# Kernel optimization log

Hardware: AMD Instinct MI355X
Metric: run time of the kernel (lower is better)

## Reference

```python
import jax, jax.numpy as jnp
import numpy as np

N = 100000      # nodes
E = 1600000     # edges (avg degree 16)
EL = 200000     # supervision (label) edges
D_IN, D_HID, D_OUT = 128, 128, 64


def setup_inputs() -> dict:
    key = jax.random.key(0)
    k = jax.random.split(key, 6)
    x = jax.random.normal(k[0], (N, D_IN), jnp.float32)
    edge_index = jax.random.randint(k[1], (2, E), 0, N, dtype=jnp.int32)
    edge_label_index = jax.random.randint(k[2], (2, EL), 0, N, dtype=jnp.int32)
    W1 = jax.random.normal(k[3], (D_IN, D_HID), jnp.float32) * (1.0 / np.sqrt(D_IN))
    b1 = jnp.zeros((D_HID,), jnp.float32)
    W2 = jax.random.normal(k[4], (D_HID, D_OUT), jnp.float32) * (1.0 / np.sqrt(D_HID))
    b2 = jnp.zeros((D_OUT,), jnp.float32)
    return {"x": x, "edge_index": edge_index, "edge_label_index": edge_label_index,
            "W1": W1, "b1": b1, "W2": W2, "b2": b2}


def gcn_layer(x, src, dst, W, b, n):
    """PyG-style GCNConv: linear -> sym-normalized scatter-add with self loops -> +bias."""
    h = x @ W                                   # [N, F]
    ones = jnp.ones(src.shape[0], h.dtype)
    deg = jax.ops.segment_sum(ones, dst, num_segments=n) + 1.0   # in-degree + self loop
    dinv = jax.lax.rsqrt(deg)                   # deg^{-1/2}
    norm = dinv[src] * dinv[dst]                # per-edge norm
    agg = jax.ops.segment_sum(h[src] * norm[:, None], dst, num_segments=n)
    agg = agg + h * (1.0 / deg)[:, None]        # self-loop contribution: dinv[i]^2
    return agg + b


def reference(x, edge_index, edge_label_index, W1, b1, W2, b2):
    src, dst = edge_index[0], edge_index[1]
    z = gcn_layer(x, src, dst, W1, b1, N)
    z = jax.nn.relu(z)                          # dropout omitted (eval mode)
    z = gcn_layer(z, src, dst, W2, b2, N)
    # decode: gather-dot over supervision edges
    return (z[edge_label_index[0]] * z[edge_label_index[1]]).sum(axis=-1)
```

## Files before the change

### kernel.cpp

```cpp
#include <hip/hip_runtime.h>
#include <stdint.h>

typedef __bf16 bf16x8 __attribute__((ext_vector_type(8)));
typedef float  floatx4 __attribute__((ext_vector_type(4)));
typedef float  floatx2 __attribute__((ext_vector_type(2)));
typedef __fp16 h2 __attribute__((ext_vector_type(2)));

__device__ __forceinline__ unsigned short f2b(float x){
    unsigned u = __float_as_uint(x);
    u = u + 0x7FFFu + ((u >> 16) & 1u);
    return (unsigned short)(u >> 16);
}
__device__ __forceinline__ float b2f(unsigned short h){
    return __uint_as_float(((unsigned)h) << 16);
}
__device__ __forceinline__ unsigned char f2f8(float x){
    int p = __builtin_amdgcn_cvt_pk_fp8_f32(x, x, 0, false);
    return (unsigned char)(p & 0xff);
}

__global__ __launch_bounds__(256) void k_scatter2(const int* __restrict__ src,
                                                  const int* __restrict__ dst,
                                                  int* __restrict__ gcur,
                                                  unsigned* __restrict__ slab,
                                                  int E_, int nbins){
    __shared__ int h[1024];
    __shared__ unsigned wbuf[4096];
    __shared__ unsigned short bbuf[4096];
    int t = threadIdx.x, blk = blockIdx.x;
    for (int i = t; i < nbins; i += 256) h[i] = 0;
    __syncthreads();
    int base = blk * 4096;
    int valid = E_ - base; if (valid > 4096) valid = 4096;
    #pragma unroll
    for (int j = 0; j < 4; j++){
        int li = (j * 256 + t) * 4;
        int e = base + li;
        if (e < E_){
            int4 d = *(const int4*)(dst + e);
            int4 s = *(const int4*)(src + e);
            wbuf[li + 0] = ((unsigned)(d.x & 127) << 25) | (unsigned)s.x;
            wbuf[li + 1] = ((unsigned)(d.y & 127) << 25) | (unsigned)s.y;
            wbuf[li + 2] = ((unsigned)(d.z & 127) << 25) | (unsigned)s.z;
            wbuf[li + 3] = ((unsigned)(d.w & 127) << 25) | (unsigned)s.w;
            bbuf[li + 0] = (unsigned short)(d.x >> 7);
            bbuf[li + 1] = (unsigned short)(d.y >> 7);
            bbuf[li + 2] = (unsigned short)(d.z >> 7);
            bbuf[li + 3] = (unsigned short)(d.w >> 7);
            atomicAdd(&h[d.x >> 7], 1);
            atomicAdd(&h[d.y >> 7], 1);
            atomicAdd(&h[d.z >> 7], 1);
            atomicAdd(&h[d.w >> 7], 1);
        }
    }
    __syncthreads();
    for (int i = t; i < nbins; i += 256){
        int hv = h[i];
        h[i] = hv ? atomicAdd(&gcur[i], hv) : 0;
    }
    __syncthreads();
    for (int i = t; i < valid; i += 256){
        int bin = bbuf[i];
        int p = atomicAdd(&h[bin], 1);
        slab[(size_t)bin * 4096 + p] = wbuf[i];
    }
}

__global__ __launch_bounds__(256) void k_binsort(const unsigned* __restrict__ slab,
                                                 const int* __restrict__ gcur,
                                                 int* __restrict__ csr,
                                                 int* __restrict__ cnt,
                                                 int* __restrict__ off,
                                                 float* __restrict__ dinv,
                                                 int n, int nbins){
    int b = blockIdx.x, t = threadIdx.x;
    __shared__ int sv[1024], sp[256];
    #pragma unroll
    for (int k = 0; k < 4; k++){
        int i = t * 4 + k;
        sv[i] = (i < nbins) ? gcur[i] : 0;
    }
    __syncthreads();
    int a0 = sv[t * 4], a1 = sv[t * 4 + 1], a2 = sv[t * 4 + 2], a3 = sv[t * 4 + 3];
    sp[t] = a0 + a1 + a2 + a3;
    __syncthreads();
    for (int o = 1; o < 256; o <<= 1){
        int v = (t >= o) ? sp[t - o] : 0;
        __syncthreads();
        sp[t] += v;
        __syncthreads();
    }
    int basep = t ? sp[t - 1] : 0;
    sv[t * 4]     = basep;
    sv[t * 4 + 1] = basep + a0;
    sv[t * 4 + 2] = basep + a0 + a1;
    sv[t * 4 + 3] = basep + a0 + a1 + a2;
    __syncthreads();
    int s0 = sv[b];
    int len = gcur[b];
    if (len > 4096) len = 4096;
    const unsigned* seg = slab + (size_t)b * 4096;
    __shared__ int cl[128], sc[128], cur[128];
    __shared__ unsigned buf[4096], outb[4096];
    if (t < 128){ cl[t] = 0; cur[t] = 0; }
    __syncthreads();
    for (int i = t; i < len; i += 256) buf[i] = seg[i];
    __syncthreads();
    for (int i = t; i < len; i += 256) atomicAdd(&cl[buf[i] >> 25], 1);
    __syncthreads();
    if (t < 128) sc[t] = cl[t];
    __syncthreads();
    for (int o = 1; o < 128; o <<= 1){
        int v = 0;
        if (t < 128 && t >= o) v = sc[t - o];
        __syncthreads();
        if (t < 128) sc[t] += v;
        __syncthreads();
    }
    for (int i = t; i < len; i += 256){
        unsigned w = buf[i];
        int nd = (int)(w >> 25);
        int p = (sc[nd] - cl[nd]) + atomicAdd(&cur[nd], 1);
        outb[p] = w & 0x1FFFFFFu;
    }
    __syncthreads();
    for (int i = t; i < len; i += 256) csr[s0 + i] = (int)outb[i];
    if (t < 128){
        int node = b * 128 + t;
        if (node < n){
            cnt[node] = cl[t];
            off[node] = s0 + (sc[t] - cl[t]);
            dinv[node] = rsqrtf((float)cl[t] + 1.0f);
        }
    }
}

__global__ __launch_bounds__(256) void k_init(const float* __restrict__ W1,
                                              const float* __restrict__ W2,
                                              unsigned short* __restrict__ wf1,
                                              unsigned* __restrict__ w2p,
                                              int* __restrict__ gcur, int nbins){
    int blk = blockIdx.x, t = threadIdx.x;
    if (blk == 24){
        for (int i = t; i < nbins; i += 256) gcur[i] = 0;
        return;
    }
    int f = blk * 256 + t;
    if (f < 2048){
        int lane = f & 63;
        int ctkc = f >> 6;
        int kc = ctkc & 3, ct = ctkc >> 2;
        int col = ct * 16 + (lane & 15);
        int k0  = kc * 32 + (lane >> 4) * 8;
        unsigned short* d = wf1 + (size_t)f * 8;
        #pragma unroll
        for (int j = 0; j < 8; j++) d[j] = f2b(W1[(k0 + j) * 128 + col]);
    } else if (f < 2048 + 4096){
        int lf = f - 2048;
        int kp = lf >> 6, lane = lf & 63;
        h2 p = __builtin_amdgcn_cvt_pkrtz(W2[(2 * kp) * 64 + lane],
                                          W2[(2 * kp + 1) * 64 + lane]);
        w2p[lf] = __builtin_bit_cast(unsigned, p);
    }
}

__global__ __launch_bounds__(256) void k_gemm1(const float* __restrict__ x,
                                               const unsigned short* __restrict__ wf,
                                               const float* __restrict__ dinv,
                                               unsigned char* __restrict__ hs, int n){
    __shared__ unsigned short Wl[16384];
    __shared__ unsigned short Al[64 * 136];
    int t = threadIdx.x;
    long rowBase = (long)blockIdx.x * 64;
    {
        const uint4* s4 = (const uint4*)wf;
        uint4* d4 = (uint4*)Wl;
        #pragma unroll
        for (int i = 0; i < 8; i++) d4[t + i * 256] = s4[t + i * 256];
    }
    {
        const float4* xs = (const float4*)(x + rowBase * 128);
        #pragma unroll
        for (int k = 0; k < 8; k++){
            int i = t + k * 256;
            int r = i >> 5, c4 = (i & 31) << 2;
            float4 v = make_float4(0.f, 0.f, 0.f, 0.f);
            if (rowBase + r < n) v = xs[i];
            unsigned lo = (unsigned)f2b(v.x) | ((unsigned)f2b(v.y) << 16);
            unsigned hi = (unsigned)f2b(v.z) | ((unsigned)f2b(v.w) << 16);
            *(uint2*)&Al[r * 136 + c4] = make_uint2(lo, hi);
        }
    }
    __syncthreads();
    int w = t >> 6, lane = t & 63, lr = lane & 15, q = lane >> 4;
    floatx4 zero = {0.f, 0.f, 0.f, 0.f};
    floatx4 acc[8];
    #pragma unroll
    for (int ct = 0; ct < 8; ct++) acc[ct] = zero;
    #pragma unroll
    for (int kc = 0; kc < 4; kc++){
        bf16x8 af = *(const bf16x8*)&Al[(w * 16 + lr) * 136 + kc * 32 + q * 8];
        #pragma unroll
        for (int ct = 0; ct < 8; ct++){
            bf16x8 bf = *(const bf16x8*)&Wl[((ct * 4 + kc) * 64 + lane) * 8];
            acc[ct] = __builtin_amdgcn_mfma_f32_16x16x32_bf16(af, bf, acc[ct], 0, 0, 0);
        }
    }
    long r0 = rowBase + w * 16 + q * 4;
    #pragma unroll
    for (int r = 0; r < 4; r++){
        long row = r0 + r;
        if (row >= n) continue;
        float dv = dinv[row];
        unsigned char* orow = hs + row * 128 + lr;
        #pragma unroll
        for (int ct = 0; ct < 8; ct++) orow[ct * 16] = f2f8(acc[ct][r] * dv);
    }
}

__global__ __launch_bounds__(256) void k_agg1g2(const unsigned char* __restrict__ hs,
                                                const int* __restrict__ off,
                                                const int* __restrict__ cnt,
                                                const int* __restrict__ csr,
                                                const float* __restrict__ dinv,
                                                const float* __restrict__ b1,
                                                const unsigned* __restrict__ w2p,
                                                unsigned short* __restrict__ hs2,
                                                int n, int nwaves){
    __shared__ unsigned W2l[4096];
    __shared__ unsigned zp[4][64];
    int t = threadIdx.x;
    {
        const uint4* w4 = (const uint4*)w2p;
        uint4* d4 = (uint4*)W2l;
        #pragma unroll
        for (int i = 0; i < 4; i++) d4[t + i * 256] = w4[t + i * 256];
    }
    __syncthreads();
    int wband = t >> 6, lane = t & 63;
    float2 bb = ((const float2*)b1)[lane];
    for (int wid = blockIdx.x * 4 + wband; wid < n; wid += nwaves){
        size_t i = (size_t)wid;
        int start = off[wid], c = cnt[wid];
        unsigned short v0 = *(const unsigned short*)(hs + i * 128 + lane * 2);
        floatx2 f0 = __builtin_amdgcn_cvt_pk_f32_fp8((int)v0, false);
        float a0 = f0.x, a1 = f0.y;
        int j = 0;
        for (; j + 8 <= c; j += 8){
            size_t s0 = (size_t)csr[start + j + 0];
            size_t s1 = (size_t)csr[start + j + 1];
            size_t s2 = (size_t)csr[start + j + 2];
            size_t s3 = (size_t)csr[start + j + 3];
            size_t s4 = (size_t)csr[start + j + 4];
            size_t s5 = (size_t)csr[start + j + 5];
            size_t s6 = (size_t)csr[start + j + 6];
            size_t s7 = (size_t)csr[start + j + 7];
            unsigned short w0 = *(const unsigned short*)(hs + s0 * 128 + lane * 2);
            unsigned short w1 = *(const unsigned short*)(hs + s1 * 128 + lane * 2);
            unsigned short w2 = *(const unsigned short*)(hs + s2 * 128 + lane * 2);
            unsigned short w3 = *(const unsigned short*)(hs + s3 * 128 + lane * 2);
            unsigned short w4 = *(const unsigned short*)(hs + s4 * 128 + lane * 2);
            unsigned short w5 = *(const unsigned short*)(hs + s5 * 128 + lane * 2);
            unsigned short w6 = *(const unsigned short*)(hs + s6 * 128 + lane * 2);
            unsigned short w7 = *(const unsigned short*)(hs + s7 * 128 + lane * 2);
            floatx2 g0 = __builtin_amdgcn_cvt_pk_f32_fp8((int)w0, false);
            floatx2 g1 = __builtin_amdgcn_cvt_pk_f32_fp8((int)w1, false);
            floatx2 g2 = __builtin_amdgcn_cvt_pk_f32_fp8((int)w2, false);
            floatx2 g3 = __builtin_amdgcn_cvt_pk_f32_fp8((int)w3, false);
            floatx2 g4 = __builtin_amdgcn_cvt_pk_f32_fp8((int)w4, false);
            floatx2 g5 = __builtin_amdgcn_cvt_pk_f32_fp8((int)w5, false);
            floatx2 g6 = __builtin_amdgcn_cvt_pk_f32_fp8((int)w6, false);
            floatx2 g7 = __builtin_amdgcn_cvt_pk_f32_fp8((int)w7, false);
            a0 += g0.x; a1 += g0.y;
            a0 += g1.x; a1 += g1.y;
            a0 += g2.x; a1 += g2.y;
            a0 += g3.x; a1 += g3.y;
            a0 += g4.x; a1 += g4.y;
            a0 += g5.x; a1 += g5.y;
            a0 += g6.x; a1 += g6.y;
            a0 += g7.x; a1 += g7.y;
        }
        for (; j < c; j++){
            size_t s = (size_t)csr[start + j];
            unsigned short v = *(const unsigned short*)(hs + s * 128 + lane * 2);
            floatx2 g = __builtin_amdgcn_cvt_pk_f32_fp8((int)v, false);
            a0 += g.x; a1 += g.y;
        }
        float dv = dinv[wid];
        float z0 = fmaxf(fmaf(dv, a0, bb.x), 0.f);
        float z1 = fmaxf(fmaf(dv, a1, bb.y), 0.f);
        zp[wband][lane] = __builtin_bit_cast(unsigned, __builtin_amdgcn_cvt_pkrtz(z0, z1));
        float acc0 = 0.f, acc1 = 0.f;
        #pragma unroll 8
        for (int kp = 0; kp < 64; kp += 2){
            h2 wa = __builtin_bit_cast(h2, W2l[kp * 64 + lane]);
            h2 wb = __builtin_bit_cast(h2, W2l[(kp + 1) * 64 + lane]);
            h2 za = __builtin_bit_cast(h2, zp[wband][kp]);
            h2 zb = __builtin_bit_cast(h2, zp[wband][kp + 1]);
            acc0 = __builtin_amdgcn_fdot2(za, wa, acc0, false);
            acc1 = __builtin_amdgcn_fdot2(zb, wb, acc1, false);
        }
        hs2[((size_t)(lane >> 3) * n + i) * 8 + (lane & 7)] = f2b((acc0 + acc1) * dv);
    }
}

__global__ __launch_bounds__(256) void k_agg2(const unsigned short* __restrict__ hs,
                                              const int* __restrict__ off,
                                              const int* __restrict__ cnt,
                                              const int* __restrict__ csr,
                                              const float* __restrict__ dinv,
                                              const float* __restrict__ b2,
                                              unsigned short* __restrict__ z2,
                                              int n, int wps){
    int t = threadIdx.x;
    int slice = blockIdx.x & 7;
    int wband = t >> 6, lane = t & 63;
    int g = lane >> 3, h = lane & 7;
    const unsigned short* tab = hs + (size_t)slice * n * 8;
    float bb = b2[slice * 8 + h];
    int wIdx = (blockIdx.x >> 3) * 4 + wband;
    int nchunks = (n + 7) >> 3;
    for (int cw = wIdx; cw < nchunks; cw += wps){
        int wid = cw * 8 + g;
        if (wid < n){
            int start = off[wid];
            int c = cnt[wid];
            float dv = dinv[wid];
            float a = b2f(tab[(size_t)wid * 8 + h]);
            int j = 0;
            for (; j + 4 <= c; j += 4){
                int s0 = csr[start + j];
                int s1 = csr[start + j + 1];
                int s2 = csr[start + j + 2];
                int s3 = csr[start + j + 3];
                unsigned short w0 = tab[(size_t)s0 * 8 + h];
                unsigned short w1 = tab[(size_t)s1 * 8 + h];
                unsigned short w2 = tab[(size_t)s2 * 8 + h];
                unsigned short w3 = tab[(size_t)s3 * 8 + h];
                a += b2f(w0); a += b2f(w1); a += b2f(w2); a += b2f(w3);
            }
            for (; j < c; j++){
                int s = csr[start + j];
                a += b2f(tab[(size_t)s * 8 + h]);
            }
            z2[(size_t)wid * 64 + slice * 8 + h] = f2b(fmaf(dv, a, bb));
        }
    }
}

__global__ __launch_bounds__(256) void k_decode(const unsigned short* __restrict__ z,
                                                const int* __restrict__ es,
                                                const int* __restrict__ et,
                                                float* __restrict__ out, int m){
    int wv = (blockIdx.x * 256 + threadIdx.x) >> 6;
    int lane = threadIdx.x & 63;
    int e = wv * 4 + (lane >> 4);
    int ql = lane & 15;
    float p = 0.f;
    if (e < m){
        size_t s = (size_t)es[e], t2 = (size_t)et[e];
        uint2 vs = *(const uint2*)(z + s * 64 + ql * 4);
        uint2 vt = *(const uint2*)(z + t2 * 64 + ql * 4);
        p = b2f((unsigned short)vs.x) * b2f((unsigned short)vt.x)
          + b2f((unsigned short)(vs.x >> 16)) * b2f((unsigned short)(vt.x >> 16))
          + b2f((unsigned short)vs.y) * b2f((unsigned short)vt.y)
          + b2f((unsigned short)(vs.y >> 16)) * b2f((unsigned short)(vt.y >> 16));
    }
    #pragma unroll
    for (int o = 8; o > 0; o >>= 1) p += __shfl_xor(p, o);
    if (ql == 0 && e < m) out[e] = p;
}


extern "C" void kernel_launch(void* const* d_in, const int* in_sizes, int n_in,
                              void* d_out, int out_size, void* d_ws, size_t ws_size,
                              hipStream_t stream){
    const float* x   = (const float*)d_in[0];
    const int*   ei  = (const int*)d_in[1];
    const int*   eli = (const int*)d_in[2];
    const float* W1  = (const float*)d_in[3];
    const float* b1  = (const float*)d_in[4];
    const float* W2  = (const float*)d_in[5];
    const float* b2  = (const float*)d_in[6];
    float* out = (float*)d_out;

    int N_  = in_sizes[0] / 128;
    int E_  = in_sizes[1] / 2;
    int EL_ = in_sizes[2] / 2;
    int NBINS = (N_ + 127) >> 7;
    const int EPB = 4096;
    int NBLK = (E_ + EPB - 1) / EPB;

    char* w = (char*)d_ws;
    size_t o = 0;
    auto alloc = [&](size_t bytes) -> size_t {
        size_t r = o; o += (bytes + 511) & ~(size_t)511; return r;
    };
    size_t o_cnt  = alloc((size_t)N_ * 4);
    size_t o_off  = alloc((size_t)N_ * 4);
    size_t o_dinv = alloc((size_t)N_ * 4);
    size_t o_gcur = alloc((size_t)NBINS * 4);
    size_t o_csr  = alloc((size_t)E_ * 4);
    size_t o_wf1  = alloc(16384 * 2);
    size_t o_w2p  = alloc(4096 * 4);
    size_t o_slab = alloc((size_t)NBINS * 4096 * 4);
    size_t o_hs1  = alloc((size_t)N_ * 128);
    size_t o_hs2  = alloc((size_t)N_ * 64 * 2);

    int* cnt  = (int*)(w + o_cnt);
    int* off  = (int*)(w + o_off);
    float* dinv = (float*)(w + o_dinv);
    int* gcur = (int*)(w + o_gcur);
    int* csr  = (int*)(w + o_csr);
    unsigned short* wf1 = (unsigned short*)(w + o_wf1);
    unsigned* w2p = (unsigned*)(w + o_w2p);
    unsigned* slab = (unsigned*)(w + o_slab);
    unsigned char* hs1 = (unsigned char*)(w + o_hs1);
    unsigned short* hs2 = (unsigned short*)(w + o_hs2);
    unsigned short* z2  = (unsigned short*)(w + o_slab);

    const int AGG1_BLOCKS = 2048;
    int nwaves = AGG1_BLOCKS * 4;
    const int AGG2_BLOCKS = 2048;
    int wps = (AGG2_BLOCKS / 8) * 4;

    k_init    <<<25, 256, 0, stream>>>(W1, W2, wf1, w2p, gcur, NBINS);
    k_scatter2<<<NBLK, 256, 0, stream>>>(ei, ei + E_, gcur, slab, E_, NBINS);
    k_binsort <<<NBINS, 256, 0, stream>>>(slab, gcur, csr, cnt, off, dinv, N_, NBINS);
    k_gemm1   <<<(N_ + 63) / 64, 256, 0, stream>>>(x, wf1, dinv, hs1, N_);
    k_agg1g2  <<<AGG1_BLOCKS, 256, 0, stream>>>(hs1, off, cnt, csr, dinv, b1, w2p, hs2, N_, nwaves);
    k_agg2    <<<AGG2_BLOCKS, 256, 0, stream>>>(hs2, off, cnt, csr, dinv, b2, z2, N_, wps);
    k_decode  <<<(EL_ + 15) / 16, 256, 0, stream>>>(z2, eli, eli + EL_, out, EL_);
}
```

Before: 300.8 us.

## Split fused agg1+GEMM2 into sliced aggregation and separate MFMA GEMM2 kernel

Aggregation for layer 1 now reads a feature-sliced fp8 table (8 slices of 16 bytes per node), so each wave handles 8 nodes per slice and keeps its gathers within a smaller table that fits cache better. The per-node fdot2 second-layer transform, previously fused into aggregation, moves into a new fp16 MFMA GEMM kernel that reads a sliced z1 buffer. CSR index loads become nontemporal, and z2 and the decode step switch to the sliced layout. This adds an extra kernel launch and a round trip of z1 through memory.

```diff
diff --git a/kernel.cpp b/kernel.cpp
--- a/kernel.cpp
+++ b/kernel.cpp
@@ -2,6 +2,7 @@
 #include <stdint.h>
 
 typedef __bf16 bf16x8 __attribute__((ext_vector_type(8)));
+typedef __fp16 f16x8 __attribute__((ext_vector_type(8)));
 typedef float  floatx4 __attribute__((ext_vector_type(4)));
 typedef float  floatx2 __attribute__((ext_vector_type(2)));
 typedef __fp16 h2 __attribute__((ext_vector_type(2)));
@@ -138,10 +139,10 @@
 __global__ __launch_bounds__(256) void k_init(const float* __restrict__ W1,
                                               const float* __restrict__ W2,
                                               unsigned short* __restrict__ wf1,
-                                              unsigned* __restrict__ w2p,
+                                              unsigned short* __restrict__ wf2,
                                               int* __restrict__ gcur, int nbins){
     int blk = blockIdx.x, t = threadIdx.x;
-    if (blk == 24){
+    if (blk == 12){
         for (int i = t; i < nbins; i += 256) gcur[i] = 0;
         return;
     }
@@ -155,12 +156,19 @@
         unsigned short* d = wf1 + (size_t)f * 8;
         #pragma unroll
         for (int j = 0; j < 8; j++) d[j] = f2b(W1[(k0 + j) * 128 + col]);
-    } else if (f < 2048 + 4096){
-        int lf = f - 2048;
-        int kp = lf >> 6, lane = lf & 63;
-        h2 p = __builtin_amdgcn_cvt_pkrtz(W2[(2 * kp) * 64 + lane],
-                                          W2[(2 * kp + 1) * 64 + lane]);
-        w2p[lf] = __builtin_bit_cast(unsigned, p);
+    } else {
+        int id = f - 2048;
+        int lane = id & 63;
+        int ctkc = id >> 6;
+        int kc = ctkc & 3, ct = ctkc >> 2;
+        int col = ct * 16 + (lane & 15);
+        int k0  = kc * 32 + (lane >> 4) * 8;
+        unsigned short* d = wf2 + (size_t)id * 8;
+        #pragma unroll
+        for (int j = 0; j < 8; j++){
+            __fp16 hv = (__fp16)W2[(k0 + j) * 64 + col];
+            d[j] = __builtin_bit_cast(unsigned short, hv);
+        }
     }
 }
 
@@ -212,95 +220,124 @@
         long row = r0 + r;
         if (row >= n) continue;
         float dv = dinv[row];
-        unsigned char* orow = hs + row * 128 + lr;
-        #pragma unroll
-        for (int ct = 0; ct < 8; ct++) orow[ct * 16] = f2f8(acc[ct][r] * dv);
-    }
-}
-
-__global__ __launch_bounds__(256) void k_agg1g2(const unsigned char* __restrict__ hs,
-                                                const int* __restrict__ off,
-                                                const int* __restrict__ cnt,
-                                                const int* __restrict__ csr,
-                                                const float* __restrict__ dinv,
-                                                const float* __restrict__ b1,
-                                                const unsigned* __restrict__ w2p,
-                                                unsigned short* __restrict__ hs2,
-                                                int n, int nwaves){
-    __shared__ unsigned W2l[4096];
-    __shared__ unsigned zp[4][64];
+        #pragma unroll
+        for (int ct = 0; ct < 8; ct++)
+            hs[((size_t)ct * n + row) * 16 + lr] = f2f8(acc[ct][r] * dv);
+    }
+}
+
+__global__ __launch_bounds__(256) void k_agg1(const unsigned char* __restrict__ hs,
+                                              const int* __restrict__ off,
+                                              const int* __restrict__ cnt,
+                                              const int* __restrict__ csr,
+                                              const float* __restrict__ dinv,
+                                              const float* __restrict__ b1,
+                                              unsigned* __restrict__ z1,
+                                              int n, int wps){
     int t = threadIdx.x;
+    int slice = blockIdx.x & 7;
+    int wband = t >> 6, lane = t & 63;
+    int g = lane >> 3, h = lane & 7;
+    const unsigned char* tab = hs + (size_t)slice * n * 16;
+    unsigned* zout = z1 + (size_t)slice * n * 8;
+    float2 bb = ((const float2*)b1)[slice * 8 + h];
+    int wIdx = (blockIdx.x >> 3) * 4 + wband;
+    int nchunks = (n + 7) >> 3;
+    for (int cw = wIdx; cw < nchunks; cw += wps){
+        int wid = cw * 8 + g;
+        if (wid < n){
+            int start = off[wid];
+            int c = cnt[wid];
+            float dv = dinv[wid];
+            unsigned short u0 = *(const unsigned short*)(tab + (size_t)wid * 16 + h * 2);
+            floatx2 f0 = __builtin_amdgcn_cvt_pk_f32_fp8((int)u0, false);
+            float a0 = f0.x, a1 = f0.y;
+            int j = 0;
+            for (; j + 4 <= c; j += 4){
+                int s0 = __builtin_nontemporal_load(csr + start + j);
+                int s1 = __builtin_nontemporal_load(csr + start + j + 1);
+                int s2 = __builtin_nontemporal_load(csr + start + j + 2);
+                int s3 = __builtin_nontemporal_load(csr + start + j + 3);
+                unsigned short w0 = *(const unsigned short*)(tab + (size_t)s0 * 16 + h * 2);
+                unsigned short w1 = *(const unsigned short*)(tab + (size_t)s1 * 16 + h * 2);
+                unsigned short w2 = *(const unsigned short*)(tab + (size_t)s2 * 16 + h * 2);
+                unsigned short w3 = *(const unsigned short*)(tab + (size_t)s3 * 16 + h * 2);
+                floatx2 g0 = __builtin_amdgcn_cvt_pk_f32_fp8((int)w0, false);
+                floatx2 g1 = __builtin_amdgcn_cvt_pk_f32_fp8((int)w1, false);
+                floatx2 g2 = __builtin_amdgcn_cvt_pk_f32_fp8((int)w2, false);
+                floatx2 g3 = __builtin_amdgcn_cvt_pk_f32_fp8((int)w3, false);
+                a0 += g0.x; a1 += g0.y;
+                a0 += g1.x; a1 += g1.y;
+                a0 += g2.x; a1 += g2.y;
+                a0 += g3.x; a1 += g3.y;
+            }
+            for (; j < c; j++){
+                int s = __builtin_nontemporal_load(csr + start + j);
+                unsigned short u = *(const unsigned short*)(tab + (size_t)s * 16 + h * 2);
+                floatx2 gg = __builtin_amdgcn_cvt_pk_f32_fp8((int)u, false);
+                a0 += gg.x; a1 += gg.y;
+            }
+            float z0 = fmaxf(fmaf(dv, a0, bb.x), 0.f);
+            float z1v = fmaxf(fmaf(dv, a1, bb.y), 0.f);
+            zout[(size_t)wid * 8 + h] =
+                __builtin_bit_cast(unsigned, __builtin_amdgcn_cvt_pkrtz(z0, z1v));
+        }
+    }
+}
+
+__global__ __launch_bounds__(256) void k_gemm2(const unsigned short* __restrict__ z1,
+                                               const unsigned short* __restrict__ wf2,
+                                               const float* __restrict__ dinv,
+                                               unsigned short* __restrict__ hs2, int n){
+    __shared__ unsigned short Wl[8192];
+    __shared__ unsigned short Al[64 * 136];
+    int t = threadIdx.x;
+    long rowBase = (long)blockIdx.x * 64;
     {
-        const uint4* w4 = (const uint4*)w2p;
-        uint4* d4 = (uint4*)W2l;
-        #pragma unroll
-        for (int i = 0; i < 4; i++) d4[t + i * 256] = w4[t + i * 256];
-    }
-    __syncthreads();
-    int wband = t >> 6, lane = t & 63;
-    float2 bb = ((const float2*)b1)[lane];
-    for (int wid = blockIdx.x * 4 + wband; wid < n; wid += nwaves){
-        size_t i = (size_t)wid;
-        int start = off[wid], c = cnt[wid];
-        unsigned short v0 = *(const unsigned short*)(hs + i * 128 + lane * 2);
-        floatx2 f0 = __builtin_amdgcn_cvt_pk_f32_fp8((int)v0, false);
-        float a0 = f0.x, a1 = f0.y;
-        int j = 0;
-        for (; j + 8 <= c; j += 8){
-            size_t s0 = (size_t)csr[start + j + 0];
-            size_t s1 = (size_t)csr[start + j + 1];
-            size_t s2 = (size_t)csr[start + j + 2];
-            size_t s3 = (size_t)csr[start + j + 3];
-            size_t s4 = (size_t)csr[start + j + 4];
-            size_t s5 = (size_t)csr[start + j + 5];
-            size_t s6 = (size_t)csr[start + j + 6];
-            size_t s7 = (size_t)csr[start + j + 7];
-            unsigned short w0 = *(const unsigned short*)(hs + s0 * 128 + lane * 2);
-            unsigned short w1 = *(const unsigned short*)(hs + s1 * 128 + lane * 2);
-            unsigned short w2 = *(const unsigned short*)(hs + s2 * 128 + lane * 2);
-            unsigned short w3 = *(const unsigned short*)(hs + s3 * 128 + lane * 2);
-            unsigned short w4 = *(const unsigned short*)(hs + s4 * 128 + lane * 2);
-            unsigned short w5 = *(const unsigned short*)(hs + s5 * 128 + lane * 2);
-            unsigned short w6 = *(const unsigned short*)(hs + s6 * 128 + lane * 2);
-            unsigned short w7 = *(const unsigned short*)(hs + s7 * 128 + lane * 2);
-            floatx2 g0 = __builtin_amdgcn_cvt_pk_f32_fp8((int)w0, false);
-            floatx2 g1 = __builtin_amdgcn_cvt_pk_f32_fp8((int)w1, false);
-            floatx2 g2 = __builtin_amdgcn_cvt_pk_f32_fp8((int)w2, false);
-            floatx2 g3 = __builtin_amdgcn_cvt_pk_f32_fp8((int)w3, false);
-            floatx2 g4 = __builtin_amdgcn_cvt_pk_f32_fp8((int)w4, false);
-            floatx2 g5 = __builtin_amdgcn_cvt_pk_f32_fp8((int)w5, false);
-            floatx2 g6 = __builtin_amdgcn_cvt_pk_f32_fp8((int)w6, false);
-            floatx2 g7 = __builtin_amdgcn_cvt_pk_f32_fp8((int)w7, false);
-            a0 += g0.x; a1 += g0.y;
-            a0 += g1.x; a1 += g1.y;
-            a0 += g2.x; a1 += g2.y;
-            a0 += g3.x; a1 += g3.y;
-            a0 += g4.x; a1 += g4.y;
-            a0 += g5.x; a1 += g5.y;
-            a0 += g6.x; a1 += g6.y;
-            a0 += g7.x; a1 += g7.y;
-        }
-        for (; j < c; j++){
-            size_t s = (size_t)csr[start + j];
-            unsigned short v = *(const unsigned short*)(hs + s * 128 + lane * 2);
-            floatx2 g = __builtin_amdgcn_cvt_pk_f32_fp8((int)v, false);
-            a0 += g.x; a1 += g.y;
-        }
-        float dv = dinv[wid];
-        float z0 = fmaxf(fmaf(dv, a0, bb.x), 0.f);
-        float z1 = fmaxf(fmaf(dv, a1, bb.y), 0.f);
-        zp[wband][lane] = __builtin_bit_cast(unsigned, __builtin_amdgcn_cvt_pkrtz(z0, z1));
-        float acc0 = 0.f, acc1 = 0.f;
-        #pragma unroll 8
-        for (int kp = 0; kp < 64; kp += 2){
-            h2 wa = __builtin_bit_cast(h2, W2l[kp * 64 + lane]);
-            h2 wb = __builtin_bit_cast(h2, W2l[(kp + 1) * 64 + lane]);
-            h2 za = __builtin_bit_cast(h2, zp[wband][kp]);
-            h2 zb = __builtin_bit_cast(h2, zp[wband][kp + 1]);
-            acc0 = __builtin_amdgcn_fdot2(za, wa, acc0, false);
-            acc1 = __builtin_amdgcn_fdot2(zb, wb, acc1, false);
-        }
-        hs2[((size_t)(lane >> 3) * n + i) * 8 + (lane & 7)] = f2b((acc0 + acc1) * dv);
+        const uint4* s4 = (const uint4*)wf2;
+        uint4* d4 = (uint4*)Wl;
+        #pragma unroll
+        for (int i = 0; i < 4; i++) d4[t + i * 256] = s4[t + i * 256];
+    }
+    {
+        #pragma unroll
+        for (int k = 0; k < 4; k++){
+            int i = t + k * 256;
+            int sl = i >> 7;
+            int node = (i >> 1) & 63;
+            int hf = i & 1;
+            long row = rowBase + node;
+            uint4 v = make_uint4(0, 0, 0, 0);
+            if (row < n) v = *(const uint4*)(z1 + ((size_t)sl * n + row) * 16 + hf * 8);
+            *(uint4*)&Al[node * 136 + sl * 16 + hf * 8] = v;
+        }
+    }
+    __syncthreads();
+    int w = t >> 6, lane = t & 63, lr = lane & 15, q = lane >> 4;
+    floatx4 zero = {0.f, 0.f, 0.f, 0.f};
+    floatx4 acc[4];
+    #pragma unroll
+    for (int ct = 0; ct < 4; ct++) acc[ct] = zero;
+    #pragma unroll
+    for (int kc = 0; kc < 4; kc++){
+        f16x8 af = *(const f16x8*)&Al[(w * 16 + lr) * 136 + kc * 32 + q * 8];
+        #pragma unroll
+        for (int ct = 0; ct < 4; ct++){
+            f16x8 bf = *(const f16x8*)&Wl[((ct * 4 + kc) * 64 + lane) * 8];
+            acc[ct] = __builtin_amdgcn_mfma_f32_16x16x32_f16(af, bf, acc[ct], 0, 0, 0);
+        }
+    }
+    long r0 = rowBase + w * 16 + q * 4;
+    #pragma unroll
+    for (int r = 0; r < 4; r++){
+        long row = r0 + r;
+        if (row >= n) continue;
+        float dv = dinv[row];
+        #pragma unroll
+        for (int ct = 0; ct < 4; ct++){
+            int f = ct * 16 + lr;
+            hs2[((size_t)(f >> 3) * n + row) * 8 + (f & 7)] = f2b(acc[ct][r] * dv);
+        }
     }
 }
 
@@ -317,6 +354,7 @@
     int wband = t >> 6, lane = t & 63;
     int g = lane >> 3, h = lane & 7;
     const unsigned short* tab = hs + (size_t)slice * n * 8;
+    unsigned short* zs = z2 + (size_t)slice * n * 8;
     float bb = b2[slice * 8 + h];
     int wIdx = (blockIdx.x >> 3) * 4 + wband;
     int nchunks = (n + 7) >> 3;
@@ -329,10 +367,10 @@
             float a = b2f(tab[(size_t)wid * 8 + h]);
             int j = 0;
             for (; j + 4 <= c; j += 4){
-                int s0 = csr[start + j];
-                int s1 = csr[start + j + 1];
-                int s2 = csr[start + j + 2];
-                int s3 = csr[start + j + 3];
+                int s0 = __builtin_nontemporal_load(csr + start + j);
+                int s1 = __builtin_nontemporal_load(csr + start + j + 1);
+                int s2 = __builtin_nontemporal_load(csr + start + j + 2);
+                int s3 = __builtin_nontemporal_load(csr + start + j + 3);
                 unsigned short w0 = tab[(size_t)s0 * 8 + h];
                 unsigned short w1 = tab[(size_t)s1 * 8 + h];
                 unsigned short w2 = tab[(size_t)s2 * 8 + h];
@@ -340,10 +378,10 @@
                 a += b2f(w0); a += b2f(w1); a += b2f(w2); a += b2f(w3);
             }
             for (; j < c; j++){
-                int s = csr[start + j];
+                int s = __builtin_nontemporal_load(csr + start + j);
                 a += b2f(tab[(size_t)s * 8 + h]);
             }
-            z2[(size_t)wid * 64 + slice * 8 + h] = f2b(fmaf(dv, a, bb));
+            zs[(size_t)wid * 8 + h] = f2b(fmaf(dv, a, bb));
         }
     }
 }
@@ -351,7 +389,7 @@
 __global__ __launch_bounds__(256) void k_decode(const unsigned short* __restrict__ z,
                                                 const int* __restrict__ es,
                                                 const int* __restrict__ et,
-                                                float* __restrict__ out, int m){
+                                                float* __restrict__ out, int m, int n){
     int wv = (blockIdx.x * 256 + threadIdx.x) >> 6;
     int lane = threadIdx.x & 63;
     int e = wv * 4 + (lane >> 4);
@@ -359,8 +397,9 @@
     float p = 0.f;
     if (e < m){
         size_t s = (size_t)es[e], t2 = (size_t)et[e];
-        uint2 vs = *(const uint2*)(z + s * 64 + ql * 4);
-        uint2 vt = *(const uint2*)(z + t2 * 64 + ql * 4);
+        const unsigned short* zs = z + ((size_t)(ql >> 1) * n) * 8 + (ql & 1) * 4;
+        uint2 vs = *(const uint2*)(zs + s * 8);
+        uint2 vt = *(const uint2*)(zs + t2 * 8);
         p = b2f((unsigned short)vs.x) * b2f((unsigned short)vt.x)
           + b2f((unsigned short)(vs.x >> 16)) * b2f((unsigned short)(vt.x >> 16))
           + b2f((unsigned short)vs.y) * b2f((unsigned short)vt.y)
@@ -402,10 +441,12 @@
     size_t o_gcur = alloc((size_t)NBINS * 4);
     size_t o_csr  = alloc((size_t)E_ * 4);
     size_t o_wf1  = alloc(16384 * 2);
-    size_t o_w2p  = alloc(4096 * 4);
-    size_t o_slab = alloc((size_t)NBINS * 4096 * 4);
-    size_t o_hs1  = alloc((size_t)N_ * 128);
-    size_t o_hs2  = alloc((size_t)N_ * 64 * 2);
+    size_t o_wf2  = alloc(8192 * 2);
+    size_t szA = (size_t)NBINS * 4096 * 4;
+    size_t szZ1 = (size_t)N_ * 256;
+    if (szZ1 > szA) szA = szZ1;
+    size_t o_A = alloc(szA);
+    size_t o_B = alloc((size_t)N_ * 128);
 
     int* cnt  = (int*)(w + o_cnt);
     int* off  = (int*)(w + o_off);
@@ -413,22 +454,22 @@
     int* gcur = (int*)(w + o_gcur);
     int* csr  = (int*)(w + o_csr);
     unsigned short* wf1 = (unsigned short*)(w + o_wf1);
-    unsigned* w2p = (unsigned*)(w + o_w2p);
-    unsigned* slab = (unsigned*)(w + o_slab);
-    unsigned char* hs1 = (unsigned char*)(w + o_hs1);
-    unsigned short* hs2 = (unsigned short*)(w + o_hs2);
-    unsigned short* z2  = (unsigned short*)(w + o_slab);
-
-    const int AGG1_BLOCKS = 2048;
-    int nwaves = AGG1_BLOCKS * 4;
-    const int AGG2_BLOCKS = 2048;
-    int wps = (AGG2_BLOCKS / 8) * 4;
-
-    k_init    <<<25, 256, 0, stream>>>(W1, W2, wf1, w2p, gcur, NBINS);
+    unsigned short* wf2 = (unsigned short*)(w + o_wf2);
+    unsigned* slab = (unsigned*)(w + o_A);
+    unsigned* z1   = (unsigned*)(w + o_A);
+    unsigned short* z2 = (unsigned short*)(w + o_A);
+    unsigned char* hs1 = (unsigned char*)(w + o_B);
+    unsigned short* hs2 = (unsigned short*)(w + o_B);
+
+    const int AGG_BLOCKS = 2048;
+    int wps = (AGG_BLOCKS / 8) * 4;
+
+    k_init    <<<13, 256, 0, stream>>>(W1, W2, wf1, wf2, gcur, NBINS);
     k_scatter2<<<NBLK, 256, 0, stream>>>(ei, ei + E_, gcur, slab, E_, NBINS);
     k_binsort <<<NBINS, 256, 0, stream>>>(slab, gcur, csr, cnt, off, dinv, N_, NBINS);
     k_gemm1   <<<(N_ + 63) / 64, 256, 0, stream>>>(x, wf1, dinv, hs1, N_);
-    k_agg1g2  <<<AGG1_BLOCKS, 256, 0, stream>>>(hs1, off, cnt, csr, dinv, b1, w2p, hs2, N_, nwaves);
-    k_agg2    <<<AGG2_BLOCKS, 256, 0, stream>>>(hs2, off, cnt, csr, dinv, b2, z2, N_, wps);
-    k_decode  <<<(EL_ + 15) / 16, 256, 0, stream>>>(z2, eli, eli + EL_, out, EL_);
-}
+    k_agg1    <<<AGG_BLOCKS, 256, 0, stream>>>(hs1, off, cnt, csr, dinv, b1, z1, N_, wps);
+    k_gemm2   <<<(N_ + 63) / 64, 256, 0, stream>>>((const unsigned short*)z1, wf2, dinv, hs2, N_);
+    k_agg2    <<<AGG_BLOCKS, 256, 0, stream>>>(hs2, off, cnt, csr, dinv, b2, z2, N_, wps);
+    k_decode  <<<(EL_ + 15) / 16, 256, 0, stream>>>(z2, eli, eli + EL_, out, EL_, N_);
+}
```

Result: slower. 470.4 us (+56.4%).
